# Performance work log

Hardware: AMD Instinct MI355X
Metric: run time of the kernel (lower is better)

Reference implementation:

```python
import jax, jax.numpy as jnp
import numpy as np
from jax import lax

K = 16        # patch_size / kernel_size
S = 16        # stride
EMB = 768     # embed_dim
CIN = 3


def setup_inputs() -> dict:
    key = jax.random.key(0)
    k1, k2, k3, k4, k5 = jax.random.split(key, 5)
    B, H, W = 64, 384, 384
    pixel_values = jax.random.normal(k1, (B, CIN, H, W), jnp.float32)
    # offset conv: Conv2d(3, 2*K*K, kernel=K, stride=K); small init so offsets stay moderate
    offset_w = jax.random.normal(k2, (2 * K * K, CIN, K, K), jnp.float32) * 0.01
    offset_b = jax.random.normal(k3, (2 * K * K,), jnp.float32) * 0.01
    # deformable projection: DeformConv2d(3, 768, kernel=K, stride=K)
    proj_w = jax.random.normal(k4, (EMB, CIN, K, K), jnp.float32) * 0.02
    proj_b = jax.random.normal(k5, (EMB,), jnp.float32) * 0.02
    return {"pixel_values": pixel_values, "offset_w": offset_w, "offset_b": offset_b,
            "proj_w": proj_w, "proj_b": proj_b}


def _bilinear_gather(img, py, px):
    """img: [B,C,H,W]; py,px: [B,K,K,HO,WO] float sample coords.
    Returns [B,C,K,K,HO,WO] with zero padding outside the image (torchvision semantics)."""
    B, C, H, W = img.shape
    shp = py.shape
    y0 = jnp.floor(py); x0 = jnp.floor(px)
    wy1 = py - y0; wy0 = 1.0 - wy1
    wx1 = px - x0; wx0 = 1.0 - wx1
    imgf = img.reshape(B, C, H * W)

    def corner(yy, xx, w):
        valid = (yy >= 0) & (yy < H) & (xx >= 0) & (xx < W)
        yi = jnp.clip(yy, 0, H - 1).astype(jnp.int32)
        xi = jnp.clip(xx, 0, W - 1).astype(jnp.int32)
        idx = (yi * W + xi).reshape(B, -1)                       # [B, N]
        v = jnp.take_along_axis(imgf, idx[:, None, :], axis=2)   # [B, C, N]
        return v * (jnp.where(valid, w, 0.0)).reshape(B, 1, -1)

    val = (corner(y0, x0, wy0 * wx0) + corner(y0, x0 + 1, wy0 * wx1)
           + corner(y0 + 1, x0, wy1 * wx0) + corner(y0 + 1, x0 + 1, wy1 * wx1))
    return val.reshape((B, C) + shp[1:])


def reference(pixel_values, offset_w, offset_b, proj_w, proj_b):
    B, C, H, W = pixel_values.shape
    HO, WO = H // S, W // S
    # offset conv (dense, stride=patch, VALID padding)
    offset = lax.conv_general_dilated(pixel_values, offset_w, (S, S), 'VALID',
                                      dimension_numbers=('NCHW', 'OIHW', 'NCHW'))
    offset = offset + offset_b[None, :, None, None]              # [B, 2*K*K, HO, WO]
    off = offset.reshape(B, K * K, 2, HO, WO)
    dy = off[:, :, 0].reshape(B, K, K, HO, WO)
    dx = off[:, :, 1].reshape(B, K, K, HO, WO)
    # base sampling grid: p = (ho*S + i + dy, wo*S + j + dx)
    base_y = (jnp.arange(HO, dtype=jnp.float32) * S)[None, None, None, :, None] \
             + jnp.arange(K, dtype=jnp.float32)[None, :, None, None, None]
    base_x = (jnp.arange(WO, dtype=jnp.float32) * S)[None, None, None, None, :] \
             + jnp.arange(K, dtype=jnp.float32)[None, None, :, None, None]
    py = base_y + dy
    px = base_x + dx
    sampled = _bilinear_gather(pixel_values, py, px)             # [B, C, K, K, HO, WO]
    out = jnp.einsum('bcijhw,ocij->bohw', sampled, proj_w) + proj_b[None, :, None, None]
    # flatten(2).transpose(1,2) -> [B, HO*WO, EMB]
    return out.reshape(B, EMB, HO * WO).transpose(0, 2, 1)
```

## Files before the change

### kernel.cpp

```cpp
#include <hip/hip_runtime.h>
#include <stdint.h>

typedef __bf16 bf16x8 __attribute__((ext_vector_type(8)));
typedef float  f32x4  __attribute__((ext_vector_type(4)));

#define HH 384
#define WW 384
#define NPIX (HH*WW)
#define NC 3
#define NPATCH 576
#define EMB 768
#define PLEN 768
#define MLOC 32
#define KSTEPS 24
#define NLOC (64*576)
#define NTILES (NLOC/MLOC)
#define NT1 4
#define NT2 6
#define W1_UNITS (32*KSTEPS*64)
#define W2_UNITS (48*KSTEPS*64)
#define W2_OFF   (W1_UNITS*8)
#define PXP_OFF  ((W1_UNITS+W2_UNITS)*8)
#define NPIX_TOT (64*NPIX)
#define WBLKS  ((W1_UNITS + W2_UNITS) / 256)
#define PXBLKS (NPIX_TOT / (256*4))

__device__ __forceinline__ uint16_t f2bf(float f) {
    uint32_t u = __builtin_bit_cast(uint32_t, f);
    u += 0x7FFFu + ((u >> 16) & 1u);
    return (uint16_t)(u >> 16);
}
__device__ __forceinline__ uint32_t pk2(float a, float b) {
    return (uint32_t)f2bf(a) | ((uint32_t)f2bf(b) << 16);
}
__device__ __forceinline__ float bf2f(uint16_t u) {
    return __builtin_bit_cast(float, (uint32_t)u << 16);
}

__global__ __launch_bounds__(256)
void prepass(const float* __restrict__ offw, const float* __restrict__ projw,
             const float* __restrict__ pix, uint16_t* __restrict__ wz) {
    int b = blockIdx.x;
    if (b < WBLKS) {
        int u = b * 256 + threadIdx.x;
        const float* src;
        int uu;
        if (u < W1_UNITS) { src = offw; uu = u; }
        else              { src = projw; uu = u - W1_UNITS; }
        int lane = uu & 63;
        int t    = uu >> 6;
        int ks   = t % KSTEPS;
        int nt   = t / KSTEPS;
        int n    = nt * 16 + (lane & 15);
        int k0   = ks * 32 + (lane >> 4) * 8;
        const float4* s4 = (const float4*)(src + (size_t)n * PLEN + k0);
        float4 v0 = s4[0], v1 = s4[1];
        uint4 w;
        w.x = pk2(v0.x, v0.y); w.y = pk2(v0.z, v0.w);
        w.z = pk2(v1.x, v1.y); w.w = pk2(v1.z, v1.w);
        *(uint4*)(wz + (size_t)u * 8) = w;
    } else {
        int idx  = (b - WBLKS) * 256 + threadIdx.x;
        int base = idx * 4;
        int im = base / NPIX;
        int yx = base - im * NPIX;
        const float* p = pix + (size_t)im * NC * NPIX + yx;
        float4 c0 = *(const float4*)p;
        float4 c1 = *(const float4*)(p + NPIX);
        float4 c2 = *(const float4*)(p + 2 * NPIX);
        uint4 o0, o1;
        o0.x = pk2(c0.x, c1.x); o0.y = (uint32_t)f2bf(c2.x);
        o0.z = pk2(c0.y, c1.y); o0.w = (uint32_t)f2bf(c2.y);
        o1.x = pk2(c0.z, c1.z); o1.y = (uint32_t)f2bf(c2.z);
        o1.z = pk2(c0.w, c1.w); o1.w = (uint32_t)f2bf(c2.w);
        uint16_t* dst = wz + PXP_OFF + (size_t)base * 4;
        *(uint4*)dst       = o0;
        *(uint4*)(dst + 8) = o1;
    }
}

template<bool USE_WS>
__global__ __launch_bounds__(512, 4)
void fused_kernel(const float* __restrict__ pix,
                  const float* __restrict__ offw,
                  const float* __restrict__ offb,
                  const float* __restrict__ projw,
                  const float* __restrict__ projb,
                  const uint16_t* __restrict__ wz,
                  float* __restrict__ out) {
    __shared__ __align__(16) uint16_t As[MLOC][PLEN];
    __shared__ uint32_t Offs[MLOC][256];

    const int tid  = threadIdx.x;
    const int wv   = tid >> 6;
    const int lane = tid & 63;
    const int lr   = lane & 15;
    const int lg   = lane >> 4;
    const int sw0  = (lr & 7) << 3;
    const int even = ((lane & 1) == 0);

    int bid = (int)blockIdx.x;
    const int tile = (bid & 7) * 144 + (bid >> 3);

    const int loc0 = tile * MLOC;
    const int bimg = loc0 / NPATCH;
    const int p0   = loc0 - bimg * NPATCH;
    const float*    __restrict__ pb  = pix + (size_t)bimg * NC * NPIX;
    const uint16_t* __restrict__ pxp = wz + PXP_OFF + (size_t)bimg * NPIX * 4;

    #pragma unroll
    for (int uu = 0; uu < 6; ++uu) {
        int unit = tid + uu * 512;
        int loc  = unit / 96;
        int k8   = (unit - loc * 96) * 8;
        int c  = k8 >> 8;
        int i  = (k8 >> 4) & 15;
        int j  = k8 & 15;
        int p  = p0 + loc;
        int ho = p / 24;
        int wo = p - ho * 24;
        const float* g = pb + ((size_t)c * HH + ho * 16 + i) * WW + wo * 16 + j;
        float4 v0 = *(const float4*)g;
        float4 v1 = *(const float4*)(g + 4);
        uint4 w;
        w.x = pk2(v0.x, v0.y); w.y = pk2(v0.z, v0.w);
        w.z = pk2(v1.x, v1.y); w.w = pk2(v1.z, v1.w);
        *(uint4*)&As[loc][k8 ^ ((loc & 7) << 3)] = w;
    }

    auto ldb1 = [&](int ntg, int ks) -> bf16x8 {
        if (USE_WS) {
            return *(const bf16x8*)(wz + ((size_t)((ntg * KSTEPS + ks) * 64 + lane)) * 8);
        } else {
            int n = ntg * 16 + lr;
            const float4* s4 = (const float4*)(offw + (size_t)n * PLEN + ks * 32 + lg * 8);
            float4 v0 = s4[0], v1 = s4[1];
            uint4 uq = {pk2(v0.x,v0.y), pk2(v0.z,v0.w), pk2(v1.x,v1.y), pk2(v1.z,v1.w)};
            return __builtin_bit_cast(bf16x8, uq);
        }
    };
    bf16x8 b1a[NT1], b1b[NT1];
    #pragma unroll
    for (int nt = 0; nt < NT1; ++nt) b1a[nt] = ldb1(wv * NT1 + nt, 0);
    __syncthreads();

    f32x4 acc1[2][NT1];
    #pragma unroll
    for (int nt = 0; nt < NT1; ++nt) {
        float bz = offb[(wv * NT1 + nt) * 16 + lr];
        f32x4 z = {bz, bz, bz, bz};
        acc1[0][nt] = z; acc1[1][nt] = z;
    }
    #pragma unroll 1
    for (int ks2 = 0; ks2 < KSTEPS / 2; ++ks2) {
        const int ks0 = ks2 * 2;
        {
            #pragma unroll
            for (int nt = 0; nt < NT1; ++nt) b1b[nt] = ldb1(wv * NT1 + nt, ks0 + 1);
            int ke = (ks0 * 32 + lg * 8) ^ sw0;
            bf16x8 a0 = *(const bf16x8*)&As[lr][ke];
            bf16x8 a1 = *(const bf16x8*)&As[16 + lr][ke];
            __builtin_amdgcn_s_setprio(1);
            #pragma unroll
            for (int nt = 0; nt < NT1; ++nt) {
                acc1[0][nt] = __builtin_amdgcn_mfma_f32_16x16x32_bf16(a0, b1a[nt], acc1[0][nt], 0, 0, 0);
                acc1[1][nt] = __builtin_amdgcn_mfma_f32_16x16x32_bf16(a1, b1a[nt], acc1[1][nt], 0, 0, 0);
            }
            __builtin_amdgcn_s_setprio(0);
        }
        {
            int ksn = (ks0 + 2 < KSTEPS) ? ks0 + 2 : 0;
            #pragma unroll
            for (int nt = 0; nt < NT1; ++nt) b1a[nt] = ldb1(wv * NT1 + nt, ksn);
            int ke = ((ks0 + 1) * 32 + lg * 8) ^ sw0;
            bf16x8 a0 = *(const bf16x8*)&As[lr][ke];
            bf16x8 a1 = *(const bf16x8*)&As[16 + lr][ke];
            __builtin_amdgcn_s_setprio(1);
            #pragma unroll
            for (int nt = 0; nt < NT1; ++nt) {
                acc1[0][nt] = __builtin_amdgcn_mfma_f32_16x16x32_bf16(a0, b1b[nt], acc1[0][nt], 0, 0, 0);
                acc1[1][nt] = __builtin_amdgcn_mfma_f32_16x16x32_bf16(a1, b1b[nt], acc1[1][nt], 0, 0, 0);
            }
            __builtin_amdgcn_s_setprio(0);
        }
    }

    #pragma unroll
    for (int nt = 0; nt < NT1; ++nt)
      #pragma unroll
      for (int mt = 0; mt < 2; ++mt)
        #pragma unroll
        for (int r = 0; r < 4; ++r) {
            float v  = acc1[mt][nt][r];
            float pv = __shfl_xor(v, 1);
            if ((nt < 2) == (even != 0)) {
                int s   = nt & 1;
                int loc = mt * 16 + lg * 4 + r;
                int q   = (wv * NT1 + (even ? 0 : 2) + s) * 8 + (lr >> 1);
                float dy = even ? v  : pv;
                float dx = even ? pv : v;
                Offs[loc][q] = pk2(dy, dx);
            }
        }
    __syncthreads();

    {
        #pragma unroll
        for (int li = 0; li < 4; ++li) {
            const int L  = wv * 4 + li;
            const int p  = p0 + L;
            const int ho = p / 24;
            const int wo = p - ho * 24;
            const int swl = (L & 7) << 3;
            const int by = ho * 16;
            const int bx = wo * 16;
            #pragma unroll
            for (int s4 = 0; s4 < 4; ++s4) {
                const int q  = s4 * 64 + lane;
                const int qi = q >> 4;
                const int qj = q & 15;
                uint32_t od = Offs[L][q];
                float dy = bf2f((uint16_t)od);
                float dx = bf2f((uint16_t)(od >> 16));
                float py = (float)(by + qi) + dy;
                float px = (float)(bx + qj) + dx;
                float y0f = floorf(py), x0f = floorf(px);
                float wy1 = py - y0f, wy0 = 1.f - wy1;
                float wx1 = px - x0f, wx0 = 1.f - wx1;
                int y0 = (int)y0f, x0 = (int)x0f;
                float s0 = 0.f, s1 = 0.f, s2 = 0.f;
                #pragma unroll
                for (int cy = 0; cy < 2; ++cy) {
                    int yy = y0 + cy;
                    if ((unsigned)yy < (unsigned)HH) {
                        float wy = cy ? wy1 : wy0;
                        #pragma unroll
                        for (int cx = 0; cx < 2; ++cx) {
                            int xx = x0 + cx;
                            if ((unsigned)xx < (unsigned)WW) {
                                float w = wy * (cx ? wx1 : wx0);
                                float v0, v1, v2;
                                if (USE_WS) {
                                    uint2 d = *(const uint2*)(pxp + ((size_t)yy * WW + xx) * 4);
                                    v0 = bf2f((uint16_t)d.x);
                                    v1 = bf2f((uint16_t)(d.x >> 16));
                                    v2 = bf2f((uint16_t)d.y);
                                } else {
                                    const float* cp = pb + yy * WW + xx;
                                    v0 = cp[0]; v1 = cp[NPIX]; v2 = cp[2 * NPIX];
                                }
                                s0 += w * v0; s1 += w * v1; s2 += w * v2;
                            }
                        }
                    }
                }
                As[L][(      q) ^ swl] = f2bf(s0);
                As[L][(256 + q) ^ swl] = f2bf(s1);
                As[L][(512 + q) ^ swl] = f2bf(s2);
            }
        }
    }

    auto ldb2 = [&](int ntg, int ks) -> bf16x8 {
        if (USE_WS) {
            return *(const bf16x8*)(wz + W2_OFF + ((size_t)((ntg * KSTEPS + ks) * 64 + lane)) * 8);
        } else {
            int n = ntg * 16 + lr;
            const float4* s4 = (const float4*)(projw + (size_t)n * PLEN + ks * 32 + lg * 8);
            float4 v0 = s4[0], v1 = s4[1];
            uint4 uq = {pk2(v0.x,v0.y), pk2(v0.z,v0.w), pk2(v1.x,v1.y), pk2(v1.z,v1.w)};
            return __builtin_bit_cast(bf16x8, uq);
        }
    };
    bf16x8 b2a[NT2], b2b[NT2];
    #pragma unroll
    for (int nt = 0; nt < NT2; ++nt) b2a[nt] = ldb2(wv * NT2 + nt, 0);
    __syncthreads();

    f32x4 acc2[2][NT2];
    #pragma unroll
    for (int nt = 0; nt < NT2; ++nt) {
        float bz = projb[(wv * NT2 + nt) * 16 + lr];
        f32x4 z = {bz, bz, bz, bz};
        acc2[0][nt] = z; acc2[1][nt] = z;
    }
    #pragma unroll 1
    for (int ks2 = 0; ks2 < KSTEPS / 2; ++ks2) {
        const int ks0 = ks2 * 2;
        {
            #pragma unroll
            for (int nt = 0; nt < NT2; ++nt) b2b[nt] = ldb2(wv * NT2 + nt, ks0 + 1);
            int ke = (ks0 * 32 + lg * 8) ^ sw0;
            bf16x8 a0 = *(const bf16x8*)&As[lr][ke];
            bf16x8 a1 = *(const bf16x8*)&As[16 + lr][ke];
            __builtin_amdgcn_s_setprio(1);
            #pragma unroll
            for (int nt = 0; nt < NT2; ++nt) {
                acc2[0][nt] = __builtin_amdgcn_mfma_f32_16x16x32_bf16(a0, b2a[nt], acc2[0][nt], 0, 0, 0);
                acc2[1][nt] = __builtin_amdgcn_mfma_f32_16x16x32_bf16(a1, b2a[nt], acc2[1][nt], 0, 0, 0);
            }
            __builtin_amdgcn_s_setprio(0);
        }
        {
            int ksn = (ks0 + 2 < KSTEPS) ? ks0 + 2 : 0;
            #pragma unroll
            for (int nt = 0; nt < NT2; ++nt) b2a[nt] = ldb2(wv * NT2 + nt, ksn);
            int ke = ((ks0 + 1) * 32 + lg * 8) ^ sw0;
            bf16x8 a0 = *(const bf16x8*)&As[lr][ke];
            bf16x8 a1 = *(const bf16x8*)&As[16 + lr][ke];
            __builtin_amdgcn_s_setprio(1);
            #pragma unroll
            for (int nt = 0; nt < NT2; ++nt) {
                acc2[0][nt] = __builtin_amdgcn_mfma_f32_16x16x32_bf16(a0, b2b[nt], acc2[0][nt], 0, 0, 0);
                acc2[1][nt] = __builtin_amdgcn_mfma_f32_16x16x32_bf16(a1, b2b[nt], acc2[1][nt], 0, 0, 0);
            }
            __builtin_amdgcn_s_setprio(0);
        }
    }

    #pragma unroll
    for (int mt = 0; mt < 2; ++mt)
      #pragma unroll
      for (int r = 0; r < 4; ++r) {
        int flat = loc0 + mt * 16 + lg * 4 + r;
        float* op = out + (size_t)flat * EMB;
        #pragma unroll
        for (int nt = 0; nt < NT2; ++nt)
            op[(wv * NT2 + nt) * 16 + lr] = acc2[mt][nt][r];
      }
}

extern "C" void kernel_launch(void* const* d_in, const int* in_sizes, int n_in,
                              void* d_out, int out_size, void* d_ws, size_t ws_size,
                              hipStream_t stream) {
    const float* pix   = (const float*)d_in[0];
    const float* offw  = (const float*)d_in[1];
    const float* offb  = (const float*)d_in[2];
    const float* projw = (const float*)d_in[3];
    const float* projb = (const float*)d_in[4];
    float* out = (float*)d_out;
    uint16_t* wz = (uint16_t*)d_ws;

    const size_t ws_needed = (size_t)(W1_UNITS + W2_UNITS) * 16 + (size_t)NPIX_TOT * 8;

    if (ws_size >= ws_needed) {
        prepass<<<WBLKS + PXBLKS, 256, 0, stream>>>(offw, projw, pix, wz);
        fused_kernel<true><<<NTILES, 512, 0, stream>>>(pix, offw, offb, projw, projb, wz, out);
    } else {
        fused_kernel<false><<<NTILES, 512, 0, stream>>>(pix, offw, offb, projw, projb, wz, out);
    }
}
```

Before: 214.7 us.

## Alias offset buffer into A tile LDS and load patches from packed pixels

Result: slower. 730.8 us (+240.3%).

```diff
diff --git a/kernel.cpp b/kernel.cpp
--- a/kernel.cpp
+++ b/kernel.cpp
@@ -80,7 +80,7 @@
 }
 
 template<bool USE_WS>
-__global__ __launch_bounds__(512, 4)
+__global__ __launch_bounds__(512, 6)
 void fused_kernel(const float* __restrict__ pix,
                   const float* __restrict__ offw,
                   const float* __restrict__ offb,
@@ -89,7 +89,6 @@
                   const uint16_t* __restrict__ wz,
                   float* __restrict__ out) {
     __shared__ __align__(16) uint16_t As[MLOC][PLEN];
-    __shared__ uint32_t Offs[MLOC][256];
 
     const int tid  = threadIdx.x;
     const int wv   = tid >> 6;
@@ -108,24 +107,48 @@
     const float*    __restrict__ pb  = pix + (size_t)bimg * NC * NPIX;
     const uint16_t* __restrict__ pxp = wz + PXP_OFF + (size_t)bimg * NPIX * 4;
 
-    #pragma unroll
-    for (int uu = 0; uu < 6; ++uu) {
-        int unit = tid + uu * 512;
-        int loc  = unit / 96;
-        int k8   = (unit - loc * 96) * 8;
-        int c  = k8 >> 8;
-        int i  = (k8 >> 4) & 15;
-        int j  = k8 & 15;
-        int p  = p0 + loc;
-        int ho = p / 24;
-        int wo = p - ho * 24;
-        const float* g = pb + ((size_t)c * HH + ho * 16 + i) * WW + wo * 16 + j;
-        float4 v0 = *(const float4*)g;
-        float4 v1 = *(const float4*)(g + 4);
-        uint4 w;
-        w.x = pk2(v0.x, v0.y); w.y = pk2(v0.z, v0.w);
-        w.z = pk2(v1.x, v1.y); w.w = pk2(v1.z, v1.w);
-        *(uint4*)&As[loc][k8 ^ ((loc & 7) << 3)] = w;
+    if (USE_WS) {
+        #pragma unroll
+        for (int uu = 0; uu < 8; ++uu) {
+            int unit = uu * 512 + tid;
+            int xg   = unit & 7;
+            int loc  = (unit >> 3) & 31;
+            int i    = unit >> 8;
+            int p  = p0 + loc;
+            int ho = p / 24;
+            int wo = p - ho * 24;
+            const uint16_t* g = pxp + ((size_t)(ho * 16 + i) * WW + wo * 16 + xg * 2) * 4;
+            uint4 d = *(const uint4*)g;
+            uint32_t ch0 = (d.x & 0xFFFFu) | (d.z << 16);
+            uint32_t ch1 = (d.x >> 16)     | (d.z & 0xFFFF0000u);
+            uint32_t ch2 = (d.y & 0xFFFFu) | (d.w << 16);
+            int k   = i * 16 + xg * 2;
+            int swl = (loc & 7) << 3;
+            uint32_t* row = (uint32_t*)&As[loc][0];
+            row[((      k) ^ swl) >> 1] = ch0;
+            row[((256 + k) ^ swl) >> 1] = ch1;
+            row[((512 + k) ^ swl) >> 1] = ch2;
+        }
+    } else {
+        #pragma unroll
+        for (int uu = 0; uu < 6; ++uu) {
+            int unit = tid + uu * 512;
+            int loc  = unit / 96;
+            int k8   = (unit - loc * 96) * 8;
+            int c  = k8 >> 8;
+            int i  = (k8 >> 4) & 15;
+            int j  = k8 & 15;
+            int p  = p0 + loc;
+            int ho = p / 24;
+            int wo = p - ho * 24;
+            const float* g = pb + ((size_t)c * HH + ho * 16 + i) * WW + wo * 16 + j;
+            float4 v0 = *(const float4*)g;
+            float4 v1 = *(const float4*)(g + 4);
+            uint4 w;
+            w.x = pk2(v0.x, v0.y); w.y = pk2(v0.z, v0.w);
+            w.z = pk2(v1.x, v1.y); w.w = pk2(v1.z, v1.w);
+            *(uint4*)&As[loc][k8 ^ ((loc & 7) << 3)] = w;
+        }
     }
 
     auto ldb1 = [&](int ntg, int ks) -> bf16x8 {
@@ -184,6 +207,7 @@
             __builtin_amdgcn_s_setprio(0);
         }
     }
+    __syncthreads();
 
     #pragma unroll
     for (int nt = 0; nt < NT1; ++nt)
@@ -199,7 +223,7 @@
                 int q   = (wv * NT1 + (even ? 0 : 2) + s) * 8 + (lr >> 1);
                 float dy = even ? v  : pv;
                 float dx = even ? pv : v;
-                Offs[loc][q] = pk2(dy, dx);
+                ((uint32_t*)&As[loc][0])[q] = pk2(dy, dx);
             }
         }
     __syncthreads();
@@ -214,12 +238,17 @@
             const int swl = (L & 7) << 3;
             const int by = ho * 16;
             const int bx = wo * 16;
+            const uint32_t* rowu = (const uint32_t*)&As[L][0];
+            uint32_t od0 = rowu[       lane];
+            uint32_t od1 = rowu[ 64 +  lane];
+            uint32_t od2 = rowu[128 +  lane];
+            uint32_t od3 = rowu[192 +  lane];
             #pragma unroll
             for (int s4 = 0; s4 < 4; ++s4) {
                 const int q  = s4 * 64 + lane;
                 const int qi = q >> 4;
                 const int qj = q & 15;
-                uint32_t od = Offs[L][q];
+                uint32_t od = (s4 == 0) ? od0 : (s4 == 1) ? od1 : (s4 == 2) ? od2 : od3;
                 float dy = bf2f((uint16_t)od);
                 float dx = bf2f((uint16_t)(od >> 16));
                 float py = (float)(by + qi) + dy;
```
